# Performance work log

Measured on AMD Instinct MI355X. Metric: run time of the kernel, lower is better.

## Reference

```python
import jax, jax.numpy as jnp
import numpy as np

GRID = 8          # 8x8 lattice -> L = 64 sites
L = GRID * GRID
PW = 3            # 3x3 plaquettes -> plaquette_size = 9
N_PLAQ = L
LOCAL_DIM = 2
M = 128
BATCH = 2048


def _make_plaquettes():
    # One 3x3 plaquette per site with periodic boundaries, matching typical
    # GPSKet plaquette construction: plaquettes[i] = site indices of plaquette i.
    plqs = np.zeros((N_PLAQ, PW * PW), dtype=np.int32)
    for i in range(GRID):
        for j in range(GRID):
            p = i * GRID + j
            k = 0
            for di in range(PW):
                for dj in range(PW):
                    plqs[p, k] = ((i + di) % GRID) * GRID + ((j + dj) % GRID)
                    k += 1
    return jnp.asarray(plqs)


def setup_inputs() -> dict:
    key = jax.random.key(0)
    k1, k2 = jax.random.split(key)
    inputs = jax.random.randint(k1, (BATCH, L), 0, LOCAL_DIM, dtype=jnp.int32)
    # epsilon: (local_dim, n_plaquettes, M, plaquette_size)
    epsilon = jax.random.normal(k2, (LOCAL_DIM, N_PLAQ, M, PW * PW), dtype=jnp.float32)
    plaquettes = _make_plaquettes()
    return {"inputs": inputs, "plaquettes": plaquettes, "epsilon": epsilon}


def reference(inputs, plaquettes, epsilon):
    # inputs: (B, L) int occupancies (to_indices is identity cast)
    # plaquettes: (P, S) int site indices
    # epsilon: (D, P, M, S)
    P, S = plaquettes.shape
    occ_p = inputs[:, plaquettes]                       # (B, P, S) occupancy at each plaquette site
    eps_t = jnp.transpose(epsilon, (1, 3, 0, 2))        # (P, S, D, M)
    # gather epsilon[occ, p, :, s] for every (b, p, s) -> (B, P, S, M)
    gathered = eps_t[jnp.arange(P)[:, None], jnp.arange(S)[None, :], occ_p]
    site_prod = jnp.prod(gathered, axis=2)              # (B, P, M) product over plaquette sites
    # n_syms = 1 (no_syms): out_transformation sums over (plaquette, M, sym) axes
    return jnp.sum(site_prod, axis=(1, 2))              # (B,)
```

## Files before the change

### kernel.cpp

```cpp
#include <hip/hip_runtime.h>
#include <stdint.h>

#define PW 3
#define S 9
#define LSZ 64
#define NP 64
#define M 128
#define BATCH 2048
#define NPAT 512

__global__ __launch_bounds__(128) void build_table(
    const float* __restrict__ eps,
    float* __restrict__ G)
{
    const int p = blockIdx.x >> 2;
    const int q = blockIdx.x & 3;
    const int t = threadIdx.x;

    __shared__ float As[32][M + 4];
    __shared__ float Bs[4][M + 4];

    const int m = t;
    const float* ep = eps + (size_t)p * (M * S) + (size_t)m * S;
    const int dstride = NP * M * S;

    float e0[S], e1[S];
#pragma unroll
    for (int s = 0; s < S; ++s) {
        e0[s] = ep[s];
        e1[s] = ep[dstride + s];
    }
    float c01[4], c234[8];
#pragma unroll
    for (int i = 0; i < 4; ++i)
        c01[i] = ((i & 1) ? e1[0] : e0[0]) * ((i & 2) ? e1[1] : e0[1]);
#pragma unroll
    for (int i = 0; i < 8; ++i)
        c234[i] = ((i & 1) ? e1[2] : e0[2]) * ((i & 2) ? e1[3] : e0[3]) *
                  ((i & 4) ? e1[4] : e0[4]);
#pragma unroll
    for (int lo = 0; lo < 32; ++lo)
        As[lo][m] = c01[lo & 3] * c234[lo >> 2];

    const float tail = ((q & 1) ? e1[7] : e0[7]) * ((q & 2) ? e1[8] : e0[8]);
#pragma unroll
    for (int hl = 0; hl < 4; ++hl)
        Bs[hl][m] = ((hl & 1) ? e1[5] : e0[5]) * ((hl & 2) ? e1[6] : e0[6]) * tail;

    __syncthreads();

    const int lo = t & 31;
    const int hl = t >> 5;
    const float4* Arow = (const float4*)&As[lo][0];
    const float4* Brow = (const float4*)&Bs[hl][0];
    float acc = 0.f;
#pragma unroll 8
    for (int i = 0; i < M / 4; ++i) {
        float4 a = Arow[i];
        float4 b = Brow[i];
        acc += a.x * b.x + a.y * b.y + a.z * b.z + a.w * b.w;
    }
    const int hi = q * 4 + hl;
    G[p * NPAT + (hi << 5) + lo] = acc;
}

__global__ __launch_bounds__(256) void eval_kernel(
    const int* __restrict__ inputs,
    const int* __restrict__ plq,
    const float* __restrict__ G,
    float* __restrict__ out)
{
    __shared__ int splq[NP * S];
    for (int i = threadIdx.x; i < NP * S; i += 256)
        splq[i] = plq[i];
    __syncthreads();

    const int wave = threadIdx.x >> 6;
    const int lane = threadIdx.x & 63;
    const int b = blockIdx.x * 4 + wave;

    const int v = inputs[b * LSZ + lane];
    const unsigned long long mask = __ballot(v != 0);

    int pat = 0;
#pragma unroll
    for (int s = 0; s < S; ++s) {
        const int site = splq[lane * S + s];
        pat |= (int)((mask >> site) & 1ull) << s;
    }
    float val = G[lane * NPAT + pat];

#pragma unroll
    for (int off = 32; off > 0; off >>= 1)
        val += __shfl_down(val, off, 64);
    if (lane == 0) out[b] = val;
}

extern "C" void kernel_launch(void* const* d_in, const int* in_sizes, int n_in,
                              void* d_out, int out_size, void* d_ws, size_t ws_size,
                              hipStream_t stream) {
    const int*   inputs = (const int*)d_in[0];
    const int*   plq    = (const int*)d_in[1];
    const float* eps    = (const float*)d_in[2];
    float* out = (float*)d_out;
    float* G   = (float*)d_ws;

    build_table<<<NP * 4, 128, 0, stream>>>(eps, G);
    eval_kernel<<<BATCH / 4, 256, 0, stream>>>(inputs, plq, G, out);
}
```

Measured before the change: 61.41 us.

## Fuse table build and evaluation into one cooperative kernel with grid sync

Combines the table-building and batch-evaluation kernels into a single cooperative launch of 512 blocks, separated by a grid-wide barrier. The table work is split more finely, with 8 blocks per plaquette and a 4-way split of the inner product reduced with shuffles, so it uses 256 threads per block. The intent is to remove the second launch and its inter-kernel gap. In exchange it adds cooperative-launch overhead and a grid-sync cost, and it requires all 512 blocks to be co-resident on the device.

Result: slower. 125.4 us (+104.2%).

```diff
diff --git a/kernel.cpp b/kernel.cpp
--- a/kernel.cpp
+++ b/kernel.cpp
@@ -1,5 +1,8 @@
 #include <hip/hip_runtime.h>
+#include <hip/hip_cooperative_groups.h>
 #include <stdint.h>
+
+namespace cg = cooperative_groups;
 
 #define PW 3
 #define S 9
@@ -9,91 +12,112 @@
 #define BATCH 2048
 #define NPAT 512
 
-__global__ __launch_bounds__(128) void build_table(
+#define NBLK 512
+#define NTHR 256
+
+__global__ __launch_bounds__(NTHR, 2) void fused(
+    const int*   __restrict__ inputs,
+    const int*   __restrict__ plq,
     const float* __restrict__ eps,
-    float* __restrict__ G)
+    float*       __restrict__ G,
+    float*       __restrict__ out)
 {
-    const int p = blockIdx.x >> 2;
-    const int q = blockIdx.x & 3;
-    const int t = threadIdx.x;
+    __shared__ float As[32][M + 4];
+    __shared__ float Bs[2][M + 4];
+    __shared__ int   splq[NP * S];
 
-    __shared__ float As[32][M + 4];
-    __shared__ float Bs[4][M + 4];
+    const int t   = threadIdx.x;
+    const int blk = blockIdx.x;
 
-    const int m = t;
-    const float* ep = eps + (size_t)p * (M * S) + (size_t)m * S;
-    const int dstride = NP * M * S;
+    for (int i = t; i < NP * S; i += NTHR)
+        splq[i] = plq[i];
 
-    float e0[S], e1[S];
+    {
+        const int p    = blk >> 3;
+        const int hp   = blk & 7;
+        const int m    = t & 127;
+        const int half = t >> 7;
+
+        const float* ep = eps + (size_t)p * (M * S) + (size_t)m * S;
+        const int dstride = NP * M * S;
+
+        float e0[S], e1[S];
 #pragma unroll
-    for (int s = 0; s < S; ++s) {
-        e0[s] = ep[s];
-        e1[s] = ep[dstride + s];
+        for (int s = 0; s < S; ++s) {
+            e0[s] = ep[s];
+            e1[s] = ep[dstride + s];
+        }
+
+        float c01[4], c234[8];
+#pragma unroll
+        for (int i = 0; i < 4; ++i)
+            c01[i] = ((i & 1) ? e1[0] : e0[0]) * ((i & 2) ? e1[1] : e0[1]);
+#pragma unroll
+        for (int i = 0; i < 8; ++i)
+            c234[i] = ((i & 1) ? e1[2] : e0[2]) * ((i & 2) ? e1[3] : e0[3]) *
+                      ((i & 4) ? e1[4] : e0[4]);
+
+        if (half == 0) {
+#pragma unroll
+            for (int lo = 0; lo < 16; ++lo)
+                As[lo][m] = c01[lo & 3] * c234[lo >> 2];
+            const float t678 = ((hp & 1) ? e1[6] : e0[6]) *
+                               ((hp & 2) ? e1[7] : e0[7]) *
+                               ((hp & 4) ? e1[8] : e0[8]);
+            Bs[0][m] = e0[5] * t678;
+            Bs[1][m] = e1[5] * t678;
+        } else {
+#pragma unroll
+            for (int lo = 16; lo < 32; ++lo)
+                As[lo][m] = c01[lo & 3] * c234[lo >> 2];
+        }
+        __syncthreads();
+
+        const int pat = t >> 2;
+        const int c   = t & 3;
+        const int lo  = pat & 31;
+        const int hb  = pat >> 5;
+        const float4* Arow = (const float4*)&As[lo][32 * c];
+        const float4* Brow = (const float4*)&Bs[hb][32 * c];
+        float acc = 0.f;
+#pragma unroll
+        for (int i = 0; i < 8; ++i) {
+            float4 a = Arow[i];
+            float4 b = Brow[i];
+            acc += a.x * b.x + a.y * b.y + a.z * b.z + a.w * b.w;
+        }
+        acc += __shfl_xor(acc, 1, 64);
+        acc += __shfl_xor(acc, 2, 64);
+        if (c == 0) {
+            const int hi = 2 * hp + hb;
+            G[p * NPAT + (hi << 5) + lo] = acc;
+        }
     }
-    float c01[4], c234[8];
+
+    __threadfence();
+    cg::this_grid().sync();
+
+    {
+        const int wave = t >> 6;
+        const int lane = t & 63;
+        const int b = blk * 4 + wave;
+
+        const int v = inputs[b * LSZ + lane];
+        const unsigned long long mask = __ballot(v != 0);
+
+        int pat = 0;
 #pragma unroll
-    for (int i = 0; i < 4; ++i)
-        c01[i] = ((i & 1) ? e1[0] : e0[0]) * ((i & 2) ? e1[1] : e0[1]);
-#pragma unroll
-    for (int i = 0; i < 8; ++i)
-        c234[i] = ((i & 1) ? e1[2] : e0[2]) * ((i & 2) ? e1[3] : e0[3]) *
-                  ((i & 4) ? e1[4] : e0[4]);
-#pragma unroll
-    for (int lo = 0; lo < 32; ++lo)
-        As[lo][m] = c01[lo & 3] * c234[lo >> 2];
-
-    const float tail = ((q & 1) ? e1[7] : e0[7]) * ((q & 2) ? e1[8] : e0[8]);
-#pragma unroll
-    for (int hl = 0; hl < 4; ++hl)
-        Bs[hl][m] = ((hl & 1) ? e1[5] : e0[5]) * ((hl & 2) ? e1[6] : e0[6]) * tail;
-
-    __syncthreads();
-
-    const int lo = t & 31;
-    const int hl = t >> 5;
-    const float4* Arow = (const float4*)&As[lo][0];
-    const float4* Brow = (const float4*)&Bs[hl][0];
-    float acc = 0.f;
-#pragma unroll 8
-    for (int i = 0; i < M / 4; ++i) {
-        float4 a = Arow[i];
-        float4 b = Brow[i];
-        acc += a.x * b.x + a.y * b.y + a.z * b.z + a.w * b.w;
-    }
-    const int hi = q * 4 + hl;
-    G[p * NPAT + (hi << 5) + lo] = acc;
-}
-
-__global__ __launch_bounds__(256) void eval_kernel(
-    const int* __restrict__ inputs,
-    const int* __restrict__ plq,
-    const float* __restrict__ G,
-    float* __restrict__ out)
-{
-    __shared__ int splq[NP * S];
-    for (int i = threadIdx.x; i < NP * S; i += 256)
-        splq[i] = plq[i];
-    __syncthreads();
-
-    const int wave = threadIdx.x >> 6;
-    const int lane = threadIdx.x & 63;
-    const int b = blockIdx.x * 4 + wave;
-
-    const int v = inputs[b * LSZ + lane];
-    const unsigned long long mask = __ballot(v != 0);
-
-    int pat = 0;
-#pragma unroll
-    for (int s = 0; s < S; ++s) {
-        const int site = splq[lane * S + s];
-        pat |= (int)((mask >> site) & 1ull) << s;
-    }
-    float val = G[lane * NPAT + pat];
+        for (int s = 0; s < S; ++s) {
+            const int site = splq[lane * S + s];
+            pat |= (int)((mask >> site) & 1ull) << s;
+        }
+        float val = G[lane * NPAT + pat];
 
 #pragma unroll
-    for (int off = 32; off > 0; off >>= 1)
-        val += __shfl_down(val, off, 64);
-    if (lane == 0) out[b] = val;
+        for (int off = 32; off > 0; off >>= 1)
+            val += __shfl_down(val, off, 64);
+        if (lane == 0) out[b] = val;
+    }
 }
 
 extern "C" void kernel_launch(void* const* d_in, const int* in_sizes, int n_in,
@@ -105,6 +129,8 @@
     float* out = (float*)d_out;
     float* G   = (float*)d_ws;
 
-    build_table<<<NP * 4, 128, 0, stream>>>(eps, G);
-    eval_kernel<<<BATCH / 4, 256, 0, stream>>>(inputs, plq, G, out);
+    void* args[] = { (void*)&inputs, (void*)&plq, (void*)&eps,
+                     (void*)&G, (void*)&out };
+    hipLaunchCooperativeKernel((const void*)fused, dim3(NBLK), dim3(NTHR),
+                               args, 0, stream);
 }
```
